# Kernel optimization log

Measured on AMD Instinct MI355X. Metric: run time of the kernel, lower is better.

## Reference

```python
import jax, jax.numpy as jnp
import numpy as np

N = 100000        # num_nodes
F_IN = 512        # node_features
F_OUT = 2         # GCNConv out channels (hardcoded in module)
E = 3200000       # num edges (avg degree 32)


def setup_inputs() -> dict:
    key = jax.random.key(0)
    k = jax.random.split(key, 8)
    x = jax.random.normal(k[0], (N, F_IN), dtype=jnp.float32)
    edge_list = jax.random.randint(k[1], (2, E), 0, N, dtype=jnp.int64)
    edge_attr = jax.random.uniform(k[2], (E,), dtype=jnp.float32)
    # GCNConv params (glorot-ish scale)
    W = jax.random.normal(k[3], (F_IN, F_OUT), dtype=jnp.float32) / np.sqrt(F_IN)
    b = jnp.zeros((F_OUT,), dtype=jnp.float32)
    # fc head: Linear(num_nodes*2, 1)
    fc_w = jax.random.normal(k[4], (N * F_OUT,), dtype=jnp.float32) / np.sqrt(N * F_OUT)
    fc_b = jnp.zeros((), dtype=jnp.float32)
    return {"x": x, "edge_list": edge_list, "edge_attr": edge_attr,
            "W": W, "b": b, "fc_w": fc_w, "fc_b": fc_b}


def reference(x, edge_list, edge_attr, W, b, fc_w, fc_b):
    n = x.shape[0]
    row, col = edge_list[0], edge_list[1]
    # --- gcn_norm with add_self_loops=True (fill weight 1.0) ---
    loop = jnp.arange(n, dtype=edge_list.dtype)
    row_f = jnp.concatenate([row, loop])
    col_f = jnp.concatenate([col, loop])
    w_f = jnp.concatenate([edge_attr, jnp.ones((n,), dtype=edge_attr.dtype)])
    deg = jax.ops.segment_sum(w_f, col_f, num_segments=n)          # [N]
    deg_inv_sqrt = jnp.where(deg > 0, jax.lax.rsqrt(jnp.maximum(deg, 1e-30)), 0.0)
    norm = deg_inv_sqrt[row_f] * w_f * deg_inv_sqrt[col_f]          # [E+N]
    # --- linear transform then propagate (source row -> target col) ---
    h = x @ W                                                       # [N, 2]
    msg = h[row_f] * norm[:, None]                                  # [E+N, 2]
    out = jax.ops.segment_sum(msg, col_f, num_segments=n) + b      # [N, 2]
    # --- head: relu, (no dropout/noise: training=False), flatten, fc, sigmoid ---
    out = jax.nn.relu(out).reshape(-1)                              # [2N]
    logit = jnp.dot(out, fc_w) + fc_b
    return jax.nn.sigmoid(logit)
```

## Files before the change

kernel.cpp:

```cpp
#include <hip/hip_runtime.h>
#include <math.h>

#define N_NODES 100000
#define F_IN    512
#define E_EDGES 3200000

#define NR   16
#define RN   6250
#define REP  16
#define CHUNK (E_EDGES / REP)


__global__ __launch_bounds__(1024) void k_deg_tiled(const int* __restrict__ col,
                                                    const float* __restrict__ w,
                                                    float* __restrict__ rep_deg) {
    __shared__ float sdeg[RN];
    int r = blockIdx.x / REP, p = blockIdx.x % REP;
    int r0 = r * RN;
    for (int j = threadIdx.x; j < RN; j += 1024) sdeg[j] = 0.0f;
    __syncthreads();
    const int*   colc = col + p * CHUNK;
    const float* wc   = w   + p * CHUNK;
    for (int e4 = threadIdx.x * 4; e4 < CHUNK; e4 += 4096) {
        int4   c4 = *(const int4*)(colc + e4);
        float4 w4 = *(const float4*)(wc + e4);
        unsigned j;
        j = (unsigned)(c4.x - r0); if (j < RN) atomicAdd(&sdeg[j], w4.x);
        j = (unsigned)(c4.y - r0); if (j < RN) atomicAdd(&sdeg[j], w4.y);
        j = (unsigned)(c4.z - r0); if (j < RN) atomicAdd(&sdeg[j], w4.z);
        j = (unsigned)(c4.w - r0); if (j < RN) atomicAdd(&sdeg[j], w4.w);
    }
    __syncthreads();
    float* out = rep_deg + (size_t)blockIdx.x * RN;
    for (int j = threadIdx.x; j < RN; j += 1024) out[j] = sdeg[j];
}

__global__ void k_dis(const float* __restrict__ rep_deg,
                      float* __restrict__ dis, float* __restrict__ logit) {
    int i = blockIdx.x * blockDim.x + threadIdx.x;
    if (i < N_NODES) {
        int r = i / RN, j = i - r * RN;
        const float* base = rep_deg + (size_t)(r * REP) * RN + j;
        float d = 1.0f;
#pragma unroll
        for (int p = 0; p < REP; ++p) d += base[p * RN];
        dis[i] = rsqrtf(d);
    }
    if (i == 0) logit[0] = 0.0f;
}

__global__ __launch_bounds__(1024) void k_prop_tiled(const int* __restrict__ row,
                                                     const int* __restrict__ col,
                                                     const float* __restrict__ w,
                                                     const float* __restrict__ dis,
                                                     const float* __restrict__ h,
                                                     float* __restrict__ rep_acc) {
    __shared__ float sacc[RN * 2];
    int r = blockIdx.x / REP, p = blockIdx.x % REP;
    int r0 = r * RN;
    for (int j = threadIdx.x; j < RN * 2; j += 1024) sacc[j] = 0.0f;
    __syncthreads();
    const int*   colc = col + p * CHUNK;
    const int*   rowc = row + p * CHUNK;
    const float* wc   = w   + p * CHUNK;
    for (int e4 = threadIdx.x * 4; e4 < CHUNK; e4 += 4096) {
        int4 c4 = *(const int4*)(colc + e4);
#pragma unroll
        for (int q = 0; q < 4; ++q) {
            int c = (&c4.x)[q];
            unsigned j = (unsigned)(c - r0);
            if (j < RN) {
                int e  = e4 + q;
                int rr = rowc[e];
                float nm = dis[rr] * wc[e] * dis[c];
                float2 hv = *(const float2*)(h + 2 * rr);
                atomicAdd(&sacc[2 * j],     hv.x * nm);
                atomicAdd(&sacc[2 * j + 1], hv.y * nm);
            }
        }
    }
    __syncthreads();
    float* out = rep_acc + (size_t)blockIdx.x * (RN * 2);
    for (int j = threadIdx.x; j < RN * 2; j += 1024) out[j] = sacc[j];
}

__global__ __launch_bounds__(256) void k_epilogue_tiled(const float* __restrict__ rep_acc,
                                                        const float* __restrict__ h,
                                                        const float* __restrict__ dis,
                                                        const float* __restrict__ b,
                                                        const float* __restrict__ fc_w,
                                                        float* __restrict__ logit) {
    int i = blockIdx.x * blockDim.x + threadIdx.x;
    float partial = 0.0f;
    if (i < N_NODES) {
        int r = i / RN, j = i - r * RN;
        const float2* base = (const float2*)rep_acc + (size_t)(r * REP) * RN + j;
        float o0 = 0.0f, o1 = 0.0f;
#pragma unroll
        for (int p = 0; p < REP; ++p) { float2 v = base[p * RN]; o0 += v.x; o1 += v.y; }
        float d2 = dis[i] * dis[i];
        o0 += h[2 * i]     * d2 + b[0];
        o1 += h[2 * i + 1] * d2 + b[1];
        o0 = fmaxf(o0, 0.0f); o1 = fmaxf(o1, 0.0f);
        partial = o0 * fc_w[2 * i] + o1 * fc_w[2 * i + 1];
    }
#pragma unroll
    for (int off = 32; off > 0; off >>= 1)
        partial += __shfl_down(partial, off, 64);
    __shared__ float sdata[4];
    int lane = threadIdx.x & 63, wid = threadIdx.x >> 6;
    if (lane == 0) sdata[wid] = partial;
    __syncthreads();
    if (threadIdx.x == 0)
        atomicAdd(logit, sdata[0] + sdata[1] + sdata[2] + sdata[3]);
}


__global__ __launch_bounds__(256) void k_gemv(const float* __restrict__ x,
                                              const float* __restrict__ W,
                                              float* __restrict__ h) {
    int row  = (blockIdx.x * blockDim.x + threadIdx.x) >> 6;
    int lane = threadIdx.x & 63;
    if (row >= N_NODES) return;
    const float* xr = x + (size_t)row * F_IN;
    float a0 = 0.0f, a1 = 0.0f;
#pragma unroll
    for (int c = 0; c < 2; ++c) {
        int k = c * 256 + lane * 4;
        float4 xv  = *(const float4*)(xr + k);
        float4 w01 = *(const float4*)(W + 2 * k);
        float4 w23 = *(const float4*)(W + 2 * k + 4);
        a0 += xv.x * w01.x + xv.y * w01.z + xv.z * w23.x + xv.w * w23.z;
        a1 += xv.x * w01.y + xv.y * w01.w + xv.z * w23.y + xv.w * w23.w;
    }
#pragma unroll
    for (int off = 32; off > 0; off >>= 1) {
        a0 += __shfl_down(a0, off, 64);
        a1 += __shfl_down(a1, off, 64);
    }
    if (lane == 0) { h[2 * row] = a0; h[2 * row + 1] = a1; }
}

__global__ void k_sigmoid(const float* __restrict__ logit,
                          const float* __restrict__ fc_b,
                          float* __restrict__ out) {
    float z = logit[0] + fc_b[0];
    out[0] = 1.0f / (1.0f + expf(-z));
}


__global__ void k_init(float* __restrict__ deg, float* __restrict__ accum,
                       float* __restrict__ logit) {
    int i = blockIdx.x * blockDim.x + threadIdx.x;
    if (i < N_NODES) {
        deg[i] = 1.0f;
        accum[2 * i] = 0.0f;
        accum[2 * i + 1] = 0.0f;
    }
    if (i == 0) logit[0] = 0.0f;
}

__global__ void k_deg(const int* __restrict__ col, const float* __restrict__ w,
                      float* __restrict__ deg) {
    int e = blockIdx.x * blockDim.x + threadIdx.x;
    if (e < E_EDGES) atomicAdd(&deg[col[e]], w[e]);
}

__global__ void k_rsqrt(float* __restrict__ deg) {
    int i = blockIdx.x * blockDim.x + threadIdx.x;
    if (i < N_NODES) deg[i] = rsqrtf(deg[i]);
}

__global__ void k_prop(const int* __restrict__ row, const int* __restrict__ col,
                       const float* __restrict__ w, const float* __restrict__ dis,
                       const float* __restrict__ h, float* __restrict__ accum) {
    int e = blockIdx.x * blockDim.x + threadIdx.x;
    if (e < E_EDGES) {
        int r = row[e], c = col[e];
        float nm = dis[r] * w[e] * dis[c];
        atomicAdd(&accum[2 * c],     h[2 * r] * nm);
        atomicAdd(&accum[2 * c + 1], h[2 * r + 1] * nm);
    }
}

__global__ __launch_bounds__(256) void k_epilogue(const float* __restrict__ accum,
                                                  const float* __restrict__ h,
                                                  const float* __restrict__ dis,
                                                  const float* __restrict__ b,
                                                  const float* __restrict__ fc_w,
                                                  float* __restrict__ logit) {
    int i = blockIdx.x * blockDim.x + threadIdx.x;
    float partial = 0.0f;
    if (i < N_NODES) {
        float d2 = dis[i] * dis[i];
        float o0 = accum[2 * i]     + h[2 * i]     * d2 + b[0];
        float o1 = accum[2 * i + 1] + h[2 * i + 1] * d2 + b[1];
        o0 = fmaxf(o0, 0.0f); o1 = fmaxf(o1, 0.0f);
        partial = o0 * fc_w[2 * i] + o1 * fc_w[2 * i + 1];
    }
#pragma unroll
    for (int off = 32; off > 0; off >>= 1)
        partial += __shfl_down(partial, off, 64);
    __shared__ float sdata[4];
    int lane = threadIdx.x & 63, wid = threadIdx.x >> 6;
    if (lane == 0) sdata[wid] = partial;
    __syncthreads();
    if (threadIdx.x == 0)
        atomicAdd(logit, sdata[0] + sdata[1] + sdata[2] + sdata[3]);
}


extern "C" void kernel_launch(void* const* d_in, const int* in_sizes, int n_in,
                              void* d_out, int out_size, void* d_ws, size_t ws_size,
                              hipStream_t stream) {
    const float* x   = (const float*)d_in[0];
    const int*   el  = (const int*)d_in[1];
    const float* ea  = (const float*)d_in[2];
    const float* W   = (const float*)d_in[3];
    const float* b   = (const float*)d_in[4];
    const float* fcw = (const float*)d_in[5];
    const float* fcb = (const float*)d_in[6];
    float*       out = (float*)d_out;

    const int* row = el;
    const int* col = el + E_EDGES;

    float* ws = (float*)d_ws;
    const int TB = 256;
    dim3 gN((N_NODES + TB - 1) / TB);
    dim3 gG((N_NODES * 64 + TB - 1) / TB);

    const size_t need_fast = (size_t)(2 * N_NODES + N_NODES +
                                      NR * REP * RN + NR * REP * RN * 2 + 64) * 4;

    if (ws_size >= need_fast) {
        float* h       = ws;
        float* dis     = ws + 2 * N_NODES;
        float* rep_deg = ws + 3 * N_NODES;
        float* rep_acc = rep_deg + (size_t)NR * REP * RN;
        float* logit   = rep_acc + (size_t)NR * REP * RN * 2;

        k_deg_tiled     <<<NR * REP, 1024, 0, stream>>>(col, ea, rep_deg);
        k_dis           <<<gN, TB, 0, stream>>>(rep_deg, dis, logit);
        k_gemv          <<<gG, TB, 0, stream>>>(x, W, h);
        k_prop_tiled    <<<NR * REP, 1024, 0, stream>>>(row, col, ea, dis, h, rep_acc);
        k_epilogue_tiled<<<gN, TB, 0, stream>>>(rep_acc, h, dis, b, fcw, logit);
        k_sigmoid       <<<1, 1, 0, stream>>>(logit, fcb, out);
    } else {
        float* deg   = ws;
        float* h     = ws + N_NODES;
        float* accum = ws + 3 * N_NODES;
        float* logit = ws + 5 * N_NODES;
        dim3 gE((E_EDGES + TB - 1) / TB);
        k_init    <<<gN, TB, 0, stream>>>(deg, accum, logit);
        k_deg     <<<gE, TB, 0, stream>>>(col, ea, deg);
        k_rsqrt   <<<gN, TB, 0, stream>>>(deg);
        k_gemv    <<<gG, TB, 0, stream>>>(x, W, h);
        k_prop    <<<gE, TB, 0, stream>>>(row, col, ea, deg, h, accum);
        k_epilogue<<<gN, TB, 0, stream>>>(accum, h, deg, b, fcw, logit);
        k_sigmoid <<<1, 1, 0, stream>>>(logit, fcb, out);
    }
}
```

Before: 467.0 us.

## Prescale features by source degree norm and double edge-chunk replication

Folds the source-side deg^-1/2 factor into the GEMV output (g = dis*h) and applies the target-side factor once per node in the epilogue. This removes two random dis gathers per edge in the propagation kernel. REP rises from 16 to 32, which doubles the block count for the tiled degree and propagation kernels but also doubles the partial-sum buffers the reduction kernels must read. The degree kernel now loads edge weights only for in-range columns instead of loading a full float4 each time.

```diff
diff --git a/kernel.cpp b/kernel.cpp
--- a/kernel.cpp
+++ b/kernel.cpp
@@ -7,7 +7,7 @@
 
 #define NR   16
 #define RN   6250
-#define REP  16
+#define REP  32
 #define CHUNK (E_EDGES / REP)
 
 
@@ -22,13 +22,12 @@
     const int*   colc = col + p * CHUNK;
     const float* wc   = w   + p * CHUNK;
     for (int e4 = threadIdx.x * 4; e4 < CHUNK; e4 += 4096) {
-        int4   c4 = *(const int4*)(colc + e4);
-        float4 w4 = *(const float4*)(wc + e4);
-        unsigned j;
-        j = (unsigned)(c4.x - r0); if (j < RN) atomicAdd(&sdeg[j], w4.x);
-        j = (unsigned)(c4.y - r0); if (j < RN) atomicAdd(&sdeg[j], w4.y);
-        j = (unsigned)(c4.z - r0); if (j < RN) atomicAdd(&sdeg[j], w4.z);
-        j = (unsigned)(c4.w - r0); if (j < RN) atomicAdd(&sdeg[j], w4.w);
+        int4 c4 = *(const int4*)(colc + e4);
+#pragma unroll
+        for (int q = 0; q < 4; ++q) {
+            unsigned j = (unsigned)((&c4.x)[q] - r0);
+            if (j < RN) atomicAdd(&sdeg[j], wc[e4 + q]);
+        }
     }
     __syncthreads();
     float* out = rep_deg + (size_t)blockIdx.x * RN;
@@ -49,76 +48,10 @@
     if (i == 0) logit[0] = 0.0f;
 }
 
-__global__ __launch_bounds__(1024) void k_prop_tiled(const int* __restrict__ row,
-                                                     const int* __restrict__ col,
-                                                     const float* __restrict__ w,
-                                                     const float* __restrict__ dis,
-                                                     const float* __restrict__ h,
-                                                     float* __restrict__ rep_acc) {
-    __shared__ float sacc[RN * 2];
-    int r = blockIdx.x / REP, p = blockIdx.x % REP;
-    int r0 = r * RN;
-    for (int j = threadIdx.x; j < RN * 2; j += 1024) sacc[j] = 0.0f;
-    __syncthreads();
-    const int*   colc = col + p * CHUNK;
-    const int*   rowc = row + p * CHUNK;
-    const float* wc   = w   + p * CHUNK;
-    for (int e4 = threadIdx.x * 4; e4 < CHUNK; e4 += 4096) {
-        int4 c4 = *(const int4*)(colc + e4);
-#pragma unroll
-        for (int q = 0; q < 4; ++q) {
-            int c = (&c4.x)[q];
-            unsigned j = (unsigned)(c - r0);
-            if (j < RN) {
-                int e  = e4 + q;
-                int rr = rowc[e];
-                float nm = dis[rr] * wc[e] * dis[c];
-                float2 hv = *(const float2*)(h + 2 * rr);
-                atomicAdd(&sacc[2 * j],     hv.x * nm);
-                atomicAdd(&sacc[2 * j + 1], hv.y * nm);
-            }
-        }
-    }
-    __syncthreads();
-    float* out = rep_acc + (size_t)blockIdx.x * (RN * 2);
-    for (int j = threadIdx.x; j < RN * 2; j += 1024) out[j] = sacc[j];
-}
-
-__global__ __launch_bounds__(256) void k_epilogue_tiled(const float* __restrict__ rep_acc,
-                                                        const float* __restrict__ h,
-                                                        const float* __restrict__ dis,
-                                                        const float* __restrict__ b,
-                                                        const float* __restrict__ fc_w,
-                                                        float* __restrict__ logit) {
-    int i = blockIdx.x * blockDim.x + threadIdx.x;
-    float partial = 0.0f;
-    if (i < N_NODES) {
-        int r = i / RN, j = i - r * RN;
-        const float2* base = (const float2*)rep_acc + (size_t)(r * REP) * RN + j;
-        float o0 = 0.0f, o1 = 0.0f;
-#pragma unroll
-        for (int p = 0; p < REP; ++p) { float2 v = base[p * RN]; o0 += v.x; o1 += v.y; }
-        float d2 = dis[i] * dis[i];
-        o0 += h[2 * i]     * d2 + b[0];
-        o1 += h[2 * i + 1] * d2 + b[1];
-        o0 = fmaxf(o0, 0.0f); o1 = fmaxf(o1, 0.0f);
-        partial = o0 * fc_w[2 * i] + o1 * fc_w[2 * i + 1];
-    }
-#pragma unroll
-    for (int off = 32; off > 0; off >>= 1)
-        partial += __shfl_down(partial, off, 64);
-    __shared__ float sdata[4];
-    int lane = threadIdx.x & 63, wid = threadIdx.x >> 6;
-    if (lane == 0) sdata[wid] = partial;
-    __syncthreads();
-    if (threadIdx.x == 0)
-        atomicAdd(logit, sdata[0] + sdata[1] + sdata[2] + sdata[3]);
-}
-
-
 __global__ __launch_bounds__(256) void k_gemv(const float* __restrict__ x,
                                               const float* __restrict__ W,
-                                              float* __restrict__ h) {
+                                              const float* __restrict__ dis,
+                                              float* __restrict__ g) {
     int row  = (blockIdx.x * blockDim.x + threadIdx.x) >> 6;
     int lane = threadIdx.x & 63;
     if (row >= N_NODES) return;
@@ -138,7 +71,75 @@
         a0 += __shfl_down(a0, off, 64);
         a1 += __shfl_down(a1, off, 64);
     }
-    if (lane == 0) { h[2 * row] = a0; h[2 * row + 1] = a1; }
+    if (lane == 0) {
+        float d = dis[row];
+        g[2 * row] = a0 * d;
+        g[2 * row + 1] = a1 * d;
+    }
+}
+
+__global__ __launch_bounds__(1024) void k_prop_tiled(const int* __restrict__ row,
+                                                     const int* __restrict__ col,
+                                                     const float* __restrict__ w,
+                                                     const float* __restrict__ g,
+                                                     float* __restrict__ rep_acc) {
+    __shared__ float sacc[RN * 2];
+    int r = blockIdx.x / REP, p = blockIdx.x % REP;
+    int r0 = r * RN;
+    for (int j = threadIdx.x; j < RN * 2; j += 1024) sacc[j] = 0.0f;
+    __syncthreads();
+    const int*   colc = col + p * CHUNK;
+    const int*   rowc = row + p * CHUNK;
+    const float* wc   = w   + p * CHUNK;
+    for (int e4 = threadIdx.x * 4; e4 < CHUNK; e4 += 4096) {
+        int4 c4 = *(const int4*)(colc + e4);
+#pragma unroll
+        for (int q = 0; q < 4; ++q) {
+            unsigned j = (unsigned)((&c4.x)[q] - r0);
+            if (j < RN) {
+                int e  = e4 + q;
+                int rr = rowc[e];
+                float we = wc[e];
+                float2 gv = *(const float2*)(g + 2 * rr);
+                atomicAdd(&sacc[2 * j],     gv.x * we);
+                atomicAdd(&sacc[2 * j + 1], gv.y * we);
+            }
+        }
+    }
+    __syncthreads();
+    float* out = rep_acc + (size_t)blockIdx.x * (RN * 2);
+    for (int j = threadIdx.x; j < RN * 2; j += 1024) out[j] = sacc[j];
+}
+
+__global__ __launch_bounds__(256) void k_epilogue_tiled(const float* __restrict__ rep_acc,
+                                                        const float* __restrict__ g,
+                                                        const float* __restrict__ dis,
+                                                        const float* __restrict__ b,
+                                                        const float* __restrict__ fc_w,
+                                                        float* __restrict__ logit) {
+    int i = blockIdx.x * blockDim.x + threadIdx.x;
+    float partial = 0.0f;
+    if (i < N_NODES) {
+        int r = i / RN, j = i - r * RN;
+        const float2* base = (const float2*)rep_acc + (size_t)(r * REP) * RN + j;
+        float o0 = 0.0f, o1 = 0.0f;
+#pragma unroll
+        for (int p = 0; p < REP; ++p) { float2 v = base[p * RN]; o0 += v.x; o1 += v.y; }
+        float d = dis[i];
+        o0 = (o0 + g[2 * i])     * d + b[0];
+        o1 = (o1 + g[2 * i + 1]) * d + b[1];
+        o0 = fmaxf(o0, 0.0f); o1 = fmaxf(o1, 0.0f);
+        partial = o0 * fc_w[2 * i] + o1 * fc_w[2 * i + 1];
+    }
+#pragma unroll
+    for (int off = 32; off > 0; off >>= 1)
+        partial += __shfl_down(partial, off, 64);
+    __shared__ float sdata[4];
+    int lane = threadIdx.x & 63, wid = threadIdx.x >> 6;
+    if (lane == 0) sdata[wid] = partial;
+    __syncthreads();
+    if (threadIdx.x == 0)
+        atomicAdd(logit, sdata[0] + sdata[1] + sdata[2] + sdata[3]);
 }
 
 __global__ void k_sigmoid(const float* __restrict__ logit,
@@ -169,6 +170,30 @@
 __global__ void k_rsqrt(float* __restrict__ deg) {
     int i = blockIdx.x * blockDim.x + threadIdx.x;
     if (i < N_NODES) deg[i] = rsqrtf(deg[i]);
+}
+
+__global__ void k_gemv_h(const float* __restrict__ x, const float* __restrict__ W,
+                         float* __restrict__ h) {
+    int row  = (blockIdx.x * blockDim.x + threadIdx.x) >> 6;
+    int lane = threadIdx.x & 63;
+    if (row >= N_NODES) return;
+    const float* xr = x + (size_t)row * F_IN;
+    float a0 = 0.0f, a1 = 0.0f;
+#pragma unroll
+    for (int c = 0; c < 2; ++c) {
+        int k = c * 256 + lane * 4;
+        float4 xv  = *(const float4*)(xr + k);
+        float4 w01 = *(const float4*)(W + 2 * k);
+        float4 w23 = *(const float4*)(W + 2 * k + 4);
+        a0 += xv.x * w01.x + xv.y * w01.z + xv.z * w23.x + xv.w * w23.z;
+        a1 += xv.x * w01.y + xv.y * w01.w + xv.z * w23.y + xv.w * w23.w;
+    }
+#pragma unroll
+    for (int off = 32; off > 0; off >>= 1) {
+        a0 += __shfl_down(a0, off, 64);
+        a1 += __shfl_down(a1, off, 64);
+    }
+    if (lane == 0) { h[2 * row] = a0; h[2 * row + 1] = a1; }
 }
 
 __global__ void k_prop(const int* __restrict__ row, const int* __restrict__ col,
@@ -230,11 +255,11 @@
     dim3 gN((N_NODES + TB - 1) / TB);
     dim3 gG((N_NODES * 64 + TB - 1) / TB);
 
-    const size_t need_fast = (size_t)(2 * N_NODES + N_NODES +
-                                      NR * REP * RN + NR * REP * RN * 2 + 64) * 4;
+    const size_t need_fast = (size_t)(3 * N_NODES +
+                                      (size_t)NR * REP * RN * 3 + 64) * 4;
 
     if (ws_size >= need_fast) {
-        float* h       = ws;
+        float* g       = ws;
         float* dis     = ws + 2 * N_NODES;
         float* rep_deg = ws + 3 * N_NODES;
         float* rep_acc = rep_deg + (size_t)NR * REP * RN;
@@ -242,9 +267,9 @@
 
         k_deg_tiled     <<<NR * REP, 1024, 0, stream>>>(col, ea, rep_deg);
         k_dis           <<<gN, TB, 0, stream>>>(rep_deg, dis, logit);
-        k_gemv          <<<gG, TB, 0, stream>>>(x, W, h);
-        k_prop_tiled    <<<NR * REP, 1024, 0, stream>>>(row, col, ea, dis, h, rep_acc);
-        k_epilogue_tiled<<<gN, TB, 0, stream>>>(rep_acc, h, dis, b, fcw, logit);
+        k_gemv          <<<gG, TB, 0, stream>>>(x, W, dis, g);
+        k_prop_tiled    <<<NR * REP, 1024, 0, stream>>>(row, col, ea, g, rep_acc);
+        k_epilogue_tiled<<<gN, TB, 0, stream>>>(rep_acc, g, dis, b, fcw, logit);
         k_sigmoid       <<<1, 1, 0, stream>>>(logit, fcb, out);
     } else {
         float* deg   = ws;
@@ -255,7 +280,7 @@
         k_init    <<<gN, TB, 0, stream>>>(deg, accum, logit);
         k_deg     <<<gE, TB, 0, stream>>>(col, ea, deg);
         k_rsqrt   <<<gN, TB, 0, stream>>>(deg);
-        k_gemv    <<<gG, TB, 0, stream>>>(x, W, h);
+        k_gemv_h  <<<gG, TB, 0, stream>>>(x, W, h);
         k_prop    <<<gE, TB, 0, stream>>>(row, col, ea, deg, h, accum);
         k_epilogue<<<gN, TB, 0, stream>>>(accum, h, deg, b, fcw, logit);
         k_sigmoid <<<1, 1, 0, stream>>>(logit, fcb, out);
```

Result: faster. 427.3 us (-8.5%).
